# Performance work log

Hardware: AMD Instinct MI355X
Metric: run time of the kernel (lower is better)

Reference implementation:

```python
import jax, jax.numpy as jnp
from jax import lax
import numpy as np
import math

B, H, W, C = 4, 32, 256, 96
EXPAND, N, R, K = 2, 16, 6, 2
DI = EXPAND * C


def setup_inputs() -> dict:
    key = jax.random.key(0)
    ks = jax.random.split(key, 10)
    x = jax.random.normal(ks[0], (B, H, W, C), jnp.float32)
    W_in = jax.random.normal(ks[1], (2 * DI, C), jnp.float32) * (C ** -0.5)
    conv_w = jax.random.normal(ks[2], (DI, 1, 3, 3), jnp.float32) * (1.0 / 3.0)
    conv_b = jnp.zeros((DI,), jnp.float32)
    x_proj_weight = jax.random.normal(ks[3], (K, R + 2 * N, DI), jnp.float32) * (DI ** -0.5)
    dt_init_std = R ** -0.5
    dt_projs_weight = jax.random.uniform(ks[4], (K, DI, R), jnp.float32, -dt_init_std, dt_init_std)
    dt_min, dt_max = 1e-3, 1e-1
    dt = jnp.exp(jax.random.uniform(ks[5], (K, DI), jnp.float32) * (math.log(dt_max) - math.log(dt_min)) + math.log(dt_min))
    dt = jnp.clip(dt, 1e-4, None)
    dt_projs_bias = dt + jnp.log(-jnp.expm1(-dt))
    A_logs = jnp.tile(jnp.log(jnp.arange(1, N + 1, dtype=jnp.float32))[None, :], (K * DI, 1))
    Ds = jnp.ones((K * DI,), jnp.float32)
    W_out = jax.random.normal(ks[6], (C, DI), jnp.float32) * (DI ** -0.5)
    return {"x": x, "W_in": W_in, "conv_w": conv_w, "conv_b": conv_b,
            "x_proj_weight": x_proj_weight, "dt_projs_weight": dt_projs_weight,
            "dt_projs_bias": dt_projs_bias, "A_logs": A_logs, "Ds": Ds, "W_out": W_out}


def reference(x, W_in, conv_w, conv_b, x_proj_weight, dt_projs_weight,
              dt_projs_bias, A_logs, Ds, W_out):
    Bb, Hh, Ww, Cc = x.shape
    DIi = conv_w.shape[0]
    Kk = x_proj_weight.shape[0]
    Nn = A_logs.shape[-1]
    Rr = dt_projs_weight.shape[-1]
    L = Hh * Ww

    # in_proj + chunk
    xz = x @ W_in.T                       # (B,H,W,2*DI)
    xc, z = xz[..., :DIi], xz[..., DIi:]
    # depthwise conv (NCHW)
    xc = jnp.transpose(xc, (0, 3, 1, 2))
    xc = lax.conv_general_dilated(xc, conv_w, (1, 1), 'SAME',
                                  dimension_numbers=('NCHW', 'OIHW', 'NCHW'),
                                  feature_group_count=DIi)
    xc = jax.nn.silu(xc + conv_b[None, :, None, None])

    # cross-scan: forward + reversed (K=2)
    xf = xc.reshape(Bb, DIi, L)
    xs = jnp.stack([xf, xf[..., ::-1]], axis=1)          # (B,K,DI,L)

    x_dbl = jnp.einsum('bkdl,kcd->bkcl', xs, x_proj_weight)
    dts_r = x_dbl[:, :, :Rr]                             # (B,K,R,L)
    Bs = x_dbl[:, :, Rr:Rr + Nn]                         # (B,K,N,L)
    Cs = x_dbl[:, :, Rr + Nn:]                           # (B,K,N,L)
    dts = jnp.einsum('bkrl,kdr->bkdl', dts_r, dt_projs_weight)

    As = -jnp.exp(A_logs).reshape(Kk, DIi, Nn)           # (K,DI,N)
    Dd = Ds.reshape(Kk, DIi)
    delta = jax.nn.softplus(dts + dt_projs_bias.reshape(1, Kk, DIi, 1))

    # sequential selective scan over L
    u_t = jnp.moveaxis(xs, -1, 0)      # (L,B,K,DI)
    d_t = jnp.moveaxis(delta, -1, 0)   # (L,B,K,DI)
    B_t = jnp.moveaxis(Bs, -1, 0)      # (L,B,K,N)
    C_t = jnp.moveaxis(Cs, -1, 0)      # (L,B,K,N)

    def step(h, inp):
        u, dlt, Bt, Ct = inp
        dA = jnp.exp(dlt[..., None] * As)                       # (B,K,DI,N)
        h = dA * h + (dlt * u)[..., None] * Bt[:, :, None, :]
        y = jnp.sum(h * Ct[:, :, None, :], axis=-1)             # (B,K,DI)
        return h, y

    h0 = jnp.zeros((Bb, Kk, DIi, Nn), x.dtype)
    _, ys = lax.scan(step, h0, (u_t, d_t, B_t, C_t))
    ys = jnp.moveaxis(ys, 0, -1)                                # (B,K,DI,L)
    ys = ys + xs * Dd[None, :, :, None]

    # un-flip reversed direction and merge
    y = ys[:, 0] + ys[:, 1][..., ::-1]                          # (B,DI,L)
    y = jnp.transpose(y.reshape(Bb, DIi, Hh, Ww), (0, 2, 3, 1)) # (B,H,W,DI)

    out = (y * jax.nn.silu(z)) @ W_out.T                        # (B,H,W,C)
    return out
```

## Files before the change

### kernel.cpp

```cpp
#include <hip/hip_runtime.h>

constexpr int Bb = 4, Hh = 32, Wd = 256, Cc = 96;
constexpr int DI = 192, Nn = 16, Rr = 6, Kk = 2;
constexpr int LL = Hh * Wd;
constexpr int ROWS = Bb * LL;
constexpr int PROJ_C = 40;
constexpr int G = 128;
constexpr int CH = LL / G;
constexpr size_t YSZ = (size_t)Bb * DI * LL;

static __device__ __forceinline__ float sigmoidf_(float v) {
  return 1.f / (1.f + __expf(-v));
}

__global__ __launch_bounds__(256) void k_xz(const float* __restrict__ x,
                                            const float* __restrict__ Win,
                                            float* __restrict__ xc,
                                            float* __restrict__ zbuf) {
  __shared__ float As[32][132];
  __shared__ float Ws[32][100];
  const int tid = threadIdx.x;
  const int row0 = blockIdx.x * 128;
  const int c0 = blockIdx.y * 96;
  const int tx = tid & 7;
  const int ty = tid >> 3;
  float acc[4][12] = {};

  for (int kc = 0; kc < 3; ++kc) {
    const int d0 = kc * 32;
    __syncthreads();
    for (int v = tid; v < 1024; v += 256) {
      const int l = v >> 3, dk4 = v & 7;
      const float4 xv =
          *(const float4*)&x[(size_t)(row0 + l) * 96 + d0 + dk4 * 4];
      As[dk4 * 4 + 0][l] = xv.x;
      As[dk4 * 4 + 1][l] = xv.y;
      As[dk4 * 4 + 2][l] = xv.z;
      As[dk4 * 4 + 3][l] = xv.w;
    }
    for (int v = tid; v < 768; v += 256) {
      const int c = v >> 3, dk4 = v & 7;
      const float4 wv =
          *(const float4*)&Win[(size_t)(c0 + c) * 96 + d0 + dk4 * 4];
      Ws[dk4 * 4 + 0][c] = wv.x;
      Ws[dk4 * 4 + 1][c] = wv.y;
      Ws[dk4 * 4 + 2][c] = wv.z;
      Ws[dk4 * 4 + 3][c] = wv.w;
    }
    __syncthreads();
    for (int dk = 0; dk < 32; ++dk) {
      const float4 a4 = *(const float4*)&As[dk][ty * 4];
      const float4 w0 = *(const float4*)&Ws[dk][tx * 12];
      const float4 w1 = *(const float4*)&Ws[dk][tx * 12 + 4];
      const float4 w2 = *(const float4*)&Ws[dk][tx * 12 + 8];
      const float av[4] = {a4.x, a4.y, a4.z, a4.w};
      const float wv[12] = {w0.x, w0.y, w0.z, w0.w, w1.x, w1.y,
                            w1.z, w1.w, w2.x, w2.y, w2.z, w2.w};
#pragma unroll
      for (int i = 0; i < 4; ++i)
#pragma unroll
        for (int j = 0; j < 12; ++j)
          acc[i][j] = fmaf(av[i], wv[j], acc[i][j]);
    }
  }

  float* dst;
  int cc0;
  if (c0 < DI) { dst = xc; cc0 = c0; }
  else         { dst = zbuf; cc0 = c0 - DI; }
#pragma unroll
  for (int i = 0; i < 4; ++i) {
    float* op = dst + (size_t)(row0 + ty * 4 + i) * DI + cc0 + tx * 12;
    *(float4*)(op + 0) = make_float4(acc[i][0], acc[i][1], acc[i][2], acc[i][3]);
    *(float4*)(op + 4) = make_float4(acc[i][4], acc[i][5], acc[i][6], acc[i][7]);
    *(float4*)(op + 8) = make_float4(acc[i][8], acc[i][9], acc[i][10], acc[i][11]);
  }
}

__global__ __launch_bounds__(256) void k_conv(const float* __restrict__ xc,
                                              const float* __restrict__ cw,
                                              const float* __restrict__ cbias,
                                              float* __restrict__ xf) {
  __shared__ float wl[9 * DI];
  __shared__ float bl[DI];
  const int tid = threadIdx.x;
  for (int v = tid; v < 9 * DI; v += 256) {
    int dd = v / 9, t = v % 9;
    wl[t * DI + dd] = cw[v];
  }
  if (tid < DI) bl[tid] = cbias[tid];
  __syncthreads();

  int gid = blockIdx.x * 256 + tid;
  int d4 = gid % 48;
  int rem = gid / 48;
  int w4 = rem % 64;
  int bh = rem / 64;
  int h = bh % Hh, b = bh / Hh;
  const int d0 = d4 * 4, w0 = w4 * 4;

  float4 c[3][6];
#pragma unroll
  for (int dr = 0; dr < 3; ++dr) {
    const int h2 = h + dr - 1;
    const bool hv = (unsigned)h2 < (unsigned)Hh;
    const int hc = hv ? h2 : h;
    const float* rp = xc + ((size_t)(b * LL + (hc << 8))) * DI + d0;
#pragma unroll
    for (int j = 0; j < 6; ++j) {
      const int wc = w0 - 1 + j;
      const bool wv = (unsigned)wc < (unsigned)Wd;
      const int wcc = wv ? wc : w0;
      float4 v = *(const float4*)&rp[(size_t)wcc * DI];
      const float m = (hv && wv) ? 1.f : 0.f;
      c[dr][j] = make_float4(v.x * m, v.y * m, v.z * m, v.w * m);
    }
  }

  float4 wv9[9];
#pragma unroll
  for (int t = 0; t < 9; ++t) wv9[t] = *(const float4*)&wl[t * DI + d0];
  const float4 bias4 = *(const float4*)&bl[d0];

#pragma unroll
  for (int wi = 0; wi < 4; ++wi) {
    float4 a = bias4;
#pragma unroll
    for (int dr = 0; dr < 3; ++dr)
#pragma unroll
      for (int dc = 0; dc < 3; ++dc) {
        const float4 vv = c[dr][wi + dc];
        const float4 ww = wv9[dr * 3 + dc];
        a.x = fmaf(vv.x, ww.x, a.x);
        a.y = fmaf(vv.y, ww.y, a.y);
        a.z = fmaf(vv.z, ww.z, a.z);
        a.w = fmaf(vv.w, ww.w, a.w);
      }
    float4 r;
    r.x = a.x * sigmoidf_(a.x);
    r.y = a.y * sigmoidf_(a.y);
    r.z = a.z * sigmoidf_(a.z);
    r.w = a.w * sigmoidf_(a.w);
    *(float4*)&xf[((size_t)(b * LL + (h << 8) + w0 + wi)) * DI + d0] = r;
  }
}

__global__ __launch_bounds__(256) void k_proj(const float* __restrict__ xf,
                                              const float* __restrict__ xpw,
                                              float* __restrict__ proj) {
  __shared__ float smem[5376];
  float* As = smem;
  float* Ws = smem + 32 * 68;
  const int tid = threadIdx.x;
  const int row0 = blockIdx.x * 64;
  const int b = row0 >> 13;
  const int l0 = row0 & (LL - 1);
  const int tx = tid & 15;
  const int ty = tid >> 4;
  float acc[4][5] = {};

  for (int kc = 0; kc < 6; ++kc) {
    const int d0 = kc * 32;
    __syncthreads();
    for (int v = tid; v < 512; v += 256) {
      const int l = v >> 3, dk4 = v & 7;
      const float4 xv =
          *(const float4*)&xf[((size_t)b * LL + l0 + l) * DI + d0 + dk4 * 4];
      As[(dk4 * 4 + 0) * 68 + l] = xv.x;
      As[(dk4 * 4 + 1) * 68 + l] = xv.y;
      As[(dk4 * 4 + 2) * 68 + l] = xv.z;
      As[(dk4 * 4 + 3) * 68 + l] = xv.w;
    }
    for (int v = tid; v < 640; v += 256) {
      const int s = v >> 3, dk4 = v & 7;
      const int k = s / 40, off = s % 40;
      float4 wv = make_float4(0.f, 0.f, 0.f, 0.f);
      if (off < 6 || off >= 8) {
        const int c = off < 6 ? off : off - 2;
        wv = *(const float4*)&xpw[(size_t)(k * 38 + c) * DI + d0 + dk4 * 4];
      }
      Ws[(dk4 * 4 + 0) * 84 + s] = wv.x;
      Ws[(dk4 * 4 + 1) * 84 + s] = wv.y;
      Ws[(dk4 * 4 + 2) * 84 + s] = wv.z;
      Ws[(dk4 * 4 + 3) * 84 + s] = wv.w;
    }
    __syncthreads();
    for (int dk = 0; dk < 32; ++dk) {
      const float4 a4 = *(const float4*)&As[dk * 68 + ty * 4];
      float w[5];
#pragma unroll
      for (int j = 0; j < 5; ++j) w[j] = Ws[dk * 84 + tx * 5 + j];
      const float av[4] = {a4.x, a4.y, a4.z, a4.w};
#pragma unroll
      for (int i = 0; i < 4; ++i)
#pragma unroll
        for (int j = 0; j < 5; ++j)
          acc[i][j] = fmaf(av[i], w[j], acc[i][j]);
    }
  }

  __syncthreads();
  float* res = smem;
#pragma unroll
  for (int i = 0; i < 4; ++i)
#pragma unroll
    for (int j = 0; j < 5; ++j)
      res[(ty * 4 + i) * 84 + tx * 5 + j] = acc[i][j];
  __syncthreads();
#pragma unroll
  for (int k = 0; k < 2; ++k) {
    float* dst = proj + ((size_t)(b * Kk + k) * LL + l0) * PROJ_C;
    for (int v = tid; v < 640; v += 256) {
      const int l = v / 10, q = v % 10;
      *(float4*)&dst[l * PROJ_C + q * 4] =
          *(const float4*)&res[l * 84 + k * 40 + q * 4];
    }
  }
}

struct St {
  float4 p0;
  float2 p1;
  float u;
  float4 Bv[4];
  float4 Cv[4];
};

template <int PASS>
static __device__ __forceinline__ void load_st(St& S,
                                               const float* __restrict__ pr,
                                               const float* __restrict__ up) {
  S.p0 = *(const float4*)pr;
  S.p1 = *(const float2*)(pr + 4);
#pragma unroll
  for (int j = 0; j < 4; ++j) S.Bv[j] = *(const float4*)(pr + 8 + 4 * j);
  if (PASS == 3) {
#pragma unroll
    for (int j = 0; j < 4; ++j) S.Cv[j] = *(const float4*)(pr + 24 + 4 * j);
  }
  S.u = *up;
}

template <int PASS>
static __device__ __forceinline__ void step_compute(
    const St& S, float (&h)[16], const float (&w6)[6], const float dbias,
    const float Dv, float& dsum, float* __restrict__ yw) {
  float vr = dbias;
  vr = fmaf(S.p0.x, w6[0], vr);
  vr = fmaf(S.p0.y, w6[1], vr);
  vr = fmaf(S.p0.z, w6[2], vr);
  vr = fmaf(S.p0.w, w6[3], vr);
  vr = fmaf(S.p1.x, w6[4], vr);
  vr = fmaf(S.p1.y, w6[5], vr);
  const float ex = __expf(vr);
  const float dlt = (vr > 20.f) ? vr : __logf(1.f + ex);
  const float E = __expf(-dlt);
  if (PASS == 1) dsum += dlt;
  const float du = dlt * S.u;
  const float E2 = E * E, E4 = E2 * E2, E8 = E4 * E4;
  const float fbs[4] = {E, E4 * E, E8 * E, E8 * E4 * E};

  if (PASS == 3) {
    float yp = 0.f, yq = 0.f;
#pragma unroll
    for (int j = 0; j < 4; ++j) {
      float f = fbs[j];
      const float4 Bj = S.Bv[j];
      const float4 Cj = S.Cv[j];
      h[4 * j + 0] = fmaf(f, h[4 * j + 0], du * Bj.x);
      yp = fmaf(h[4 * j + 0], Cj.x, yp);
      f *= E;
      h[4 * j + 1] = fmaf(f, h[4 * j + 1], du * Bj.y);
      yq = fmaf(h[4 * j + 1], Cj.y, yq);
      f *= E;
      h[4 * j + 2] = fmaf(f, h[4 * j + 2], du * Bj.z);
      yp = fmaf(h[4 * j + 2], Cj.z, yp);
      f *= E;
      h[4 * j + 3] = fmaf(f, h[4 * j + 3], du * Bj.w);
      yq = fmaf(h[4 * j + 3], Cj.w, yq);
    }
    *yw = fmaf(S.u, Dv, yp + yq);
  } else {
#pragma unroll
    for (int j = 0; j < 4; ++j) {
      float f = fbs[j];
      const float4 Bj = S.Bv[j];
      h[4 * j + 0] = fmaf(f, h[4 * j + 0], du * Bj.x);
      f *= E;
      h[4 * j + 1] = fmaf(f, h[4 * j + 1], du * Bj.y);
      f *= E;
      h[4 * j + 2] = fmaf(f, h[4 * j + 2], du * Bj.z);
      f *= E;
      h[4 * j + 3] = fmaf(f, h[4 * j + 3], du * Bj.w);
    }
  }
}

template <int PASS, int KDIR>
static __device__ __forceinline__ void scan_wave(
    const float* __restrict__ proj, const float* __restrict__ xf,
    const float* __restrict__ dtw, const float* __restrict__ dtb,
    const float* __restrict__ Dsv, const float* __restrict__ hinit,
    float* __restrict__ hend, float* __restrict__ Pst,
    float* __restrict__ yout, const int b, const int g, const int d) {
  constexpr int PRS = KDIR ? -PROJ_C : PROJ_C;
  constexpr int DIS = KDIR ? -DI : DI;
  const int kd = KDIR * DI + d;
  const int bk = b * Kk + KDIR;

  float w6[6];
#pragma unroll
  for (int r = 0; r < 6; ++r) w6[r] = dtw[kd * 6 + r];
  const float dbias = dtb[kd];
  const float Dv = (PASS == 3) ? Dsv[kd] : 0.f;

  const size_t hbase = (((size_t)(bk * G + g)) * DI + d) * Nn;
  float h[16];
  if (PASS == 1) {
#pragma unroll
    for (int n = 0; n < 16; ++n) h[n] = 0.f;
  } else {
#pragma unroll
    for (int j = 0; j < 4; ++j) {
      const float4 h4 = *(const float4*)&hinit[hbase + 4 * j];
      h[4 * j + 0] = h4.x;
      h[4 * j + 1] = h4.y;
      h[4 * j + 2] = h4.z;
      h[4 * j + 3] = h4.w;
    }
  }

  const int l0 = KDIR ? (LL - 1 - g * CH) : (g * CH);
  const float* pr = proj + ((size_t)bk * LL + l0) * PROJ_C;
  const float* up = xf + ((size_t)b * LL + l0) * DI + d;
  float* yw = yout + (size_t)KDIR * YSZ + ((size_t)b * LL + l0) * DI + d;

  float dsum = 0.f;
  St S0, S1;
  load_st<PASS>(S0, pr, up);
  pr += PRS;
  up += DIS;

  for (int t = 0; t < CH; t += 2) {
    load_st<PASS>(S1, pr, up);
    pr += PRS;
    up += DIS;
    step_compute<PASS>(S0, h, w6, dbias, Dv, dsum, yw);
    if (PASS == 3) yw += DIS;
    load_st<PASS>(S0, pr, up);
    pr += PRS;
    up += DIS;
    step_compute<PASS>(S1, h, w6, dbias, Dv, dsum, yw);
    if (PASS == 3) yw += DIS;
  }

  if (PASS == 1) {
    const float Es = __expf(-dsum);
    const float Es2 = Es * Es, Es4 = Es2 * Es2, Es8 = Es4 * Es4;
    const float qbs[4] = {Es, Es4 * Es, Es8 * Es, Es8 * Es4 * Es};
#pragma unroll
    for (int j = 0; j < 4; ++j) {
      float f = qbs[j];
      float4 pv;
      pv.x = f; f *= Es;
      pv.y = f; f *= Es;
      pv.z = f; f *= Es;
      pv.w = f;
      *(float4*)&Pst[hbase + 4 * j] = pv;
      *(float4*)&hend[hbase + 4 * j] =
          make_float4(h[4 * j], h[4 * j + 1], h[4 * j + 2], h[4 * j + 3]);
    }
  }
}

template <int PASS>
__global__ __launch_bounds__(256) void k_scan(
    const float* __restrict__ proj, const float* __restrict__ xf,
    const float* __restrict__ dtw, const float* __restrict__ dtb,
    const float* __restrict__ Dsv, const float* __restrict__ hinit,
    float* __restrict__ hend, float* __restrict__ Pst,
    float* __restrict__ yout) {
  const int lane = threadIdx.x & 63;
  const int wid = blockIdx.x * 4 + (threadIdx.x >> 6);
  const int kdir = wid & 1;
  int w2 = wid >> 1;
  const int dt3 = w2 % 3;
  w2 /= 3;
  const int g = w2 & (G - 1);
  const int b = w2 >> 7;
  const int d = dt3 * 64 + lane;

  if (kdir == 0)
    scan_wave<PASS, 0>(proj, xf, dtw, dtb, Dsv, hinit, hend, Pst, yout, b, g,
                       d);
  else
    scan_wave<PASS, 1>(proj, xf, dtw, dtb, Dsv, hinit, hend, Pst, yout, b, g,
                       d);
}

__global__ __launch_bounds__(256) void k_scan2(const float* __restrict__ hend,
                                               const float* __restrict__ Pst,
                                               float* __restrict__ hini) {
  int idx = blockIdx.x * 256 + threadIdx.x;
  int n = idx & 15;
  int rem = idx >> 4;
  int d = rem % DI;
  int bk = rem / DI;
  float carry = 0.f;
#pragma unroll 8
  for (int g = 0; g < G; ++g) {
    size_t a = (((size_t)(bk * G + g)) * DI + d) * Nn + n;
    float hv = hend[a], pv = Pst[a];
    hini[a] = carry;
    carry = fmaf(pv, carry, hv);
  }
}

__global__ __launch_bounds__(256) void k_out(const float* __restrict__ y,
                                             const float* __restrict__ zbuf,
                                             const float* __restrict__ Wout,
                                             float* __restrict__ out) {
  __shared__ float As[32][132];
  __shared__ float Ws[32][100];
  const int tid = threadIdx.x;
  const int row0 = blockIdx.x * 128;
  const int b = row0 >> 13;
  const int l0 = row0 & (LL - 1);
  const int tx = tid & 7;
  const int ty = tid >> 3;
  float acc[4][12] = {};

  for (int kc = 0; kc < 6; ++kc) {
    const int d0 = kc * 32;
    __syncthreads();
    for (int v = tid; v < 1024; v += 256) {
      const int l = v >> 3, dk4 = v & 7;
      const size_t idx = ((size_t)b * LL + l0 + l) * DI + d0 + dk4 * 4;
      const float4 zv = *(const float4*)&zbuf[idx];
      const float4 y0v = *(const float4*)&y[idx];
      const float4 y1v = *(const float4*)&y[YSZ + idx];
      As[dk4 * 4 + 0][l] = zv.x * sigmoidf_(zv.x) * (y0v.x + y1v.x);
      As[dk4 * 4 + 1][l] = zv.y * sigmoidf_(zv.y) * (y0v.y + y1v.y);
      As[dk4 * 4 + 2][l] = zv.z * sigmoidf_(zv.z) * (y0v.z + y1v.z);
      As[dk4 * 4 + 3][l] = zv.w * sigmoidf_(zv.w) * (y0v.w + y1v.w);
    }
    for (int v = tid; v < 768; v += 256) {
      const int c = v >> 3, dk4 = v & 7;
      const float4 wv = *(const float4*)&Wout[(size_t)c * DI + d0 + dk4 * 4];
      Ws[dk4 * 4 + 0][c] = wv.x;
      Ws[dk4 * 4 + 1][c] = wv.y;
      Ws[dk4 * 4 + 2][c] = wv.z;
      Ws[dk4 * 4 + 3][c] = wv.w;
    }
    __syncthreads();
    for (int dk = 0; dk < 32; ++dk) {
      const float4 a4 = *(const float4*)&As[dk][ty * 4];
      const float4 w0 = *(const float4*)&Ws[dk][tx * 12];
      const float4 w1 = *(const float4*)&Ws[dk][tx * 12 + 4];
      const float4 w2 = *(const float4*)&Ws[dk][tx * 12 + 8];
      const float av[4] = {a4.x, a4.y, a4.z, a4.w};
      const float wv[12] = {w0.x, w0.y, w0.z, w0.w, w1.x, w1.y,
                            w1.z, w1.w, w2.x, w2.y, w2.z, w2.w};
#pragma unroll
      for (int i = 0; i < 4; ++i)
#pragma unroll
        for (int j = 0; j < 12; ++j)
          acc[i][j] = fmaf(av[i], wv[j], acc[i][j]);
    }
  }

#pragma unroll
  for (int i = 0; i < 4; ++i) {
    float* op = out + ((size_t)b * LL + l0 + ty * 4 + i) * 96 + tx * 12;
    *(float4*)(op + 0) = make_float4(acc[i][0], acc[i][1], acc[i][2], acc[i][3]);
    *(float4*)(op + 4) = make_float4(acc[i][4], acc[i][5], acc[i][6], acc[i][7]);
    *(float4*)(op + 8) = make_float4(acc[i][8], acc[i][9], acc[i][10], acc[i][11]);
  }
}

extern "C" void kernel_launch(void* const* d_in, const int* in_sizes, int n_in,
                              void* d_out, int out_size, void* d_ws,
                              size_t ws_size, hipStream_t stream) {
  const float* x    = (const float*)d_in[0];
  const float* Win  = (const float*)d_in[1];
  const float* cw   = (const float*)d_in[2];
  const float* cb   = (const float*)d_in[3];
  const float* xpw  = (const float*)d_in[4];
  const float* dtw  = (const float*)d_in[5];
  const float* dtb  = (const float*)d_in[6];
  const float* Dsv  = (const float*)d_in[8];
  const float* Wout = (const float*)d_in[9];
  float* out = (float*)d_out;

  float* ws = (float*)d_ws;
  size_t o = 0;
  float* zbuf  = ws + o;  o += (size_t)ROWS * DI;
  float* xf    = ws + o;  o += (size_t)ROWS * DI;
  float* proj  = ws + o;  o += (size_t)Bb * Kk * LL * PROJ_C;
  const size_t hsz = (size_t)Bb * Kk * G * DI * Nn;
  float* hend = ws + o;  o += hsz;
  float* Pst  = ws + o;  o += hsz;
  float* hini = ws + o;  o += hsz;
  float* y    = ws + o;  o += 2 * YSZ;
  float* xc   = y;

  k_xz<<<dim3(ROWS / 128, 4), 256, 0, stream>>>(x, Win, xc, zbuf);
  k_conv<<<dim3((Bb * Hh * 64 * 48) / 256), 256, 0, stream>>>(xc, cw, cb, xf);
  k_proj<<<dim3(ROWS / 64), 256, 0, stream>>>(xf, xpw, proj);
  k_scan<1><<<dim3(Bb * Kk * G * 3 / 4), 256, 0, stream>>>(
      proj, xf, dtw, dtb, Dsv, nullptr, hend, Pst, nullptr);
  k_scan2<<<dim3((Bb * Kk * DI * Nn) / 256), 256, 0, stream>>>(hend, Pst,
                                                               hini);
  k_scan<3><<<dim3(Bb * Kk * G * 3 / 4), 256, 0, stream>>>(
      proj, xf, dtw, dtb, Dsv, hini, nullptr, nullptr, y);
  k_out<<<dim3(ROWS / 128), 256, 0, stream>>>(y, zbuf, Wout, out);
}
```

Measured before the change: 337.6 us.

## Stage scan inputs through double-buffered shared memory per 192-thread block

The chunked selective-scan kernels now run one 192-thread block per (batch, direction, chunk), with all DI channels in one block. Each block cooperatively loads 16-step sub-chunks of the projection rows and u values into double-buffered LDS with coalesced float4 loads and prefetches the next sub-chunk into registers. This replaces per-thread redundant global loads of the same proj row by every lane. Pass 1 loads only the first 24 columns. The cost is block-wide barriers every 16 steps and a smaller block size.

```diff
diff --git a/kernel.cpp b/kernel.cpp
--- a/kernel.cpp
+++ b/kernel.cpp
@@ -218,95 +218,25 @@
   }
 }
 
-struct St {
-  float4 p0;
-  float2 p1;
-  float u;
-  float4 Bv[4];
-  float4 Cv[4];
-};
-
-template <int PASS>
-static __device__ __forceinline__ void load_st(St& S,
-                                               const float* __restrict__ pr,
-                                               const float* __restrict__ up) {
-  S.p0 = *(const float4*)pr;
-  S.p1 = *(const float2*)(pr + 4);
-#pragma unroll
-  for (int j = 0; j < 4; ++j) S.Bv[j] = *(const float4*)(pr + 8 + 4 * j);
-  if (PASS == 3) {
-#pragma unroll
-    for (int j = 0; j < 4; ++j) S.Cv[j] = *(const float4*)(pr + 24 + 4 * j);
-  }
-  S.u = *up;
-}
-
-template <int PASS>
-static __device__ __forceinline__ void step_compute(
-    const St& S, float (&h)[16], const float (&w6)[6], const float dbias,
-    const float Dv, float& dsum, float* __restrict__ yw) {
-  float vr = dbias;
-  vr = fmaf(S.p0.x, w6[0], vr);
-  vr = fmaf(S.p0.y, w6[1], vr);
-  vr = fmaf(S.p0.z, w6[2], vr);
-  vr = fmaf(S.p0.w, w6[3], vr);
-  vr = fmaf(S.p1.x, w6[4], vr);
-  vr = fmaf(S.p1.y, w6[5], vr);
-  const float ex = __expf(vr);
-  const float dlt = (vr > 20.f) ? vr : __logf(1.f + ex);
-  const float E = __expf(-dlt);
-  if (PASS == 1) dsum += dlt;
-  const float du = dlt * S.u;
-  const float E2 = E * E, E4 = E2 * E2, E8 = E4 * E4;
-  const float fbs[4] = {E, E4 * E, E8 * E, E8 * E4 * E};
-
-  if (PASS == 3) {
-    float yp = 0.f, yq = 0.f;
-#pragma unroll
-    for (int j = 0; j < 4; ++j) {
-      float f = fbs[j];
-      const float4 Bj = S.Bv[j];
-      const float4 Cj = S.Cv[j];
-      h[4 * j + 0] = fmaf(f, h[4 * j + 0], du * Bj.x);
-      yp = fmaf(h[4 * j + 0], Cj.x, yp);
-      f *= E;
-      h[4 * j + 1] = fmaf(f, h[4 * j + 1], du * Bj.y);
-      yq = fmaf(h[4 * j + 1], Cj.y, yq);
-      f *= E;
-      h[4 * j + 2] = fmaf(f, h[4 * j + 2], du * Bj.z);
-      yp = fmaf(h[4 * j + 2], Cj.z, yp);
-      f *= E;
-      h[4 * j + 3] = fmaf(f, h[4 * j + 3], du * Bj.w);
-      yq = fmaf(h[4 * j + 3], Cj.w, yq);
-    }
-    *yw = fmaf(S.u, Dv, yp + yq);
-  } else {
-#pragma unroll
-    for (int j = 0; j < 4; ++j) {
-      float f = fbs[j];
-      const float4 Bj = S.Bv[j];
-      h[4 * j + 0] = fmaf(f, h[4 * j + 0], du * Bj.x);
-      f *= E;
-      h[4 * j + 1] = fmaf(f, h[4 * j + 1], du * Bj.y);
-      f *= E;
-      h[4 * j + 2] = fmaf(f, h[4 * j + 2], du * Bj.z);
-      f *= E;
-      h[4 * j + 3] = fmaf(f, h[4 * j + 3], du * Bj.w);
-    }
-  }
-}
-
 template <int PASS, int KDIR>
-static __device__ __forceinline__ void scan_wave(
+static __device__ __forceinline__ void scan_block(
+    float* __restrict__ pb, float* __restrict__ ub,
     const float* __restrict__ proj, const float* __restrict__ xf,
     const float* __restrict__ dtw, const float* __restrict__ dtb,
     const float* __restrict__ Dsv, const float* __restrict__ hinit,
     float* __restrict__ hend, float* __restrict__ Pst,
-    float* __restrict__ yout, const int b, const int g, const int d) {
-  constexpr int PRS = KDIR ? -PROJ_C : PROJ_C;
+    float* __restrict__ yout, const int b, const int g) {
+  constexpr int RC = (PASS == 3) ? PROJ_C : 24;
+  constexpr int SUB = 16;
+  constexpr int NSUB = CH / SUB;
   constexpr int DIS = KDIR ? -DI : DI;
+  const int tid = threadIdx.x;
+  const int lane = tid & 63;
+  const int wv = tid >> 6;
+  const int d = wv * 64 + lane;
   const int kd = KDIR * DI + d;
   const int bk = b * Kk + KDIR;
+  const int l0 = KDIR ? (LL - 1 - g * CH) : (g * CH);
 
   float w6[6];
 #pragma unroll
@@ -330,28 +260,113 @@
     }
   }
 
-  const int l0 = KDIR ? (LL - 1 - g * CH) : (g * CH);
-  const float* pr = proj + ((size_t)bk * LL + l0) * PROJ_C;
-  const float* up = xf + ((size_t)b * LL + l0) * DI + d;
   float* yw = yout + (size_t)KDIR * YSZ + ((size_t)b * LL + l0) * DI + d;
 
+  float4 preg = make_float4(0.f, 0.f, 0.f, 0.f);
+  float4 ureg[4];
+
+  auto span = [&](int s) {
+    return KDIR ? (l0 - SUB * s - (SUB - 1)) : (l0 + SUB * s);
+  };
+  auto issue = [&](int s) {
+    const size_t pbase = ((size_t)bk * LL + span(s)) * PROJ_C;
+    const size_t ubase = ((size_t)b * LL + span(s)) * DI;
+    if (PASS == 3) {
+      if (tid < 160) preg = *(const float4*)&proj[pbase + tid * 4];
+    } else {
+      if (tid < 96) {
+        const int i = tid / 6, c4 = tid % 6;
+        preg = *(const float4*)&proj[pbase + i * PROJ_C + c4 * 4];
+      }
+    }
+#pragma unroll
+    for (int r = 0; r < 4; ++r)
+      ureg[r] = *(const float4*)&xf[ubase + (tid + 192 * r) * 4];
+  };
+  auto commit = [&](int buf) {
+    if (PASS == 3) {
+      if (tid < 160) {
+        const int i = (tid * 4) / PROJ_C, c = (tid * 4) % PROJ_C;
+        const int li = (KDIR ? (SUB - 1 - i) : i) * RC + c;
+        *(float4*)&pb[buf * (SUB * RC) + li] = preg;
+      }
+    } else {
+      if (tid < 96) {
+        const int i = tid / 6, c = (tid % 6) * 4;
+        const int li = (KDIR ? (SUB - 1 - i) : i) * RC + c;
+        *(float4*)&pb[buf * (SUB * RC) + li] = preg;
+      }
+    }
+#pragma unroll
+    for (int r = 0; r < 4; ++r) {
+      const int f4 = tid + 192 * r;
+      const int i = f4 / 48, c = (f4 % 48) * 4;
+      const int li = (KDIR ? (SUB - 1 - i) : i) * DI + c;
+      *(float4*)&ub[buf * (SUB * DI) + li] = ureg[r];
+    }
+  };
+
   float dsum = 0.f;
-  St S0, S1;
-  load_st<PASS>(S0, pr, up);
-  pr += PRS;
-  up += DIS;
-
-  for (int t = 0; t < CH; t += 2) {
-    load_st<PASS>(S1, pr, up);
-    pr += PRS;
-    up += DIS;
-    step_compute<PASS>(S0, h, w6, dbias, Dv, dsum, yw);
-    if (PASS == 3) yw += DIS;
-    load_st<PASS>(S0, pr, up);
-    pr += PRS;
-    up += DIS;
-    step_compute<PASS>(S1, h, w6, dbias, Dv, dsum, yw);
-    if (PASS == 3) yw += DIS;
+  issue(0);
+  commit(0);
+  __syncthreads();
+  issue(1);
+
+  for (int s = 0; s < NSUB; ++s) {
+    const int cur = s & 1;
+    const float* Pb = pb + cur * (SUB * RC);
+    const float* Ub = ub + cur * (SUB * DI) + d;
+#pragma unroll
+    for (int t = 0; t < SUB; ++t) {
+      const float* P = Pb + t * RC;
+      const float u = Ub[t * DI];
+      const float4 p0 = *(const float4*)P;
+      const float2 p1 = *(const float2*)(P + 4);
+      float vr = dbias;
+      vr = fmaf(p0.x, w6[0], vr);
+      vr = fmaf(p0.y, w6[1], vr);
+      vr = fmaf(p0.z, w6[2], vr);
+      vr = fmaf(p0.w, w6[3], vr);
+      vr = fmaf(p1.x, w6[4], vr);
+      vr = fmaf(p1.y, w6[5], vr);
+      const float ex = __expf(vr);
+      const float dlt = (vr > 20.f) ? vr : __logf(1.f + ex);
+      const float E = __expf(-dlt);
+      if (PASS == 1) dsum += dlt;
+      const float du = dlt * u;
+      const float E2 = E * E, E4 = E2 * E2, E8 = E4 * E4;
+      const float fbs[4] = {E, E4 * E, E8 * E, E8 * E4 * E};
+      float yp = 0.f, yq = 0.f;
+#pragma unroll
+      for (int j = 0; j < 4; ++j) {
+        float f = fbs[j];
+        const float4 Bj = *(const float4*)(P + 8 + 4 * j);
+        h[4 * j + 0] = fmaf(f, h[4 * j + 0], du * Bj.x);
+        f *= E;
+        h[4 * j + 1] = fmaf(f, h[4 * j + 1], du * Bj.y);
+        f *= E;
+        h[4 * j + 2] = fmaf(f, h[4 * j + 2], du * Bj.z);
+        f *= E;
+        h[4 * j + 3] = fmaf(f, h[4 * j + 3], du * Bj.w);
+        if (PASS == 3) {
+          const float4 Cj = *(const float4*)(P + 24 + 4 * j);
+          yp = fmaf(h[4 * j + 0], Cj.x, yp);
+          yq = fmaf(h[4 * j + 1], Cj.y, yq);
+          yp = fmaf(h[4 * j + 2], Cj.z, yp);
+          yq = fmaf(h[4 * j + 3], Cj.w, yq);
+        }
+      }
+      if (PASS == 3) {
+        *yw = fmaf(u, Dv, yp + yq);
+        yw += DIS;
+      }
+    }
+    __syncthreads();
+    if (s + 1 < NSUB) {
+      commit((s + 1) & 1);
+      if (s + 2 < NSUB) issue(s + 2);
+      __syncthreads();
+    }
   }
 
   if (PASS == 1) {
@@ -374,28 +389,28 @@
 }
 
 template <int PASS>
-__global__ __launch_bounds__(256) void k_scan(
+__global__ __launch_bounds__(192) void k_scan(
     const float* __restrict__ proj, const float* __restrict__ xf,
     const float* __restrict__ dtw, const float* __restrict__ dtb,
     const float* __restrict__ Dsv, const float* __restrict__ hinit,
     float* __restrict__ hend, float* __restrict__ Pst,
     float* __restrict__ yout) {
-  const int lane = threadIdx.x & 63;
-  const int wid = blockIdx.x * 4 + (threadIdx.x >> 6);
-  const int kdir = wid & 1;
-  int w2 = wid >> 1;
-  const int dt3 = w2 % 3;
-  w2 /= 3;
-  const int g = w2 & (G - 1);
-  const int b = w2 >> 7;
-  const int d = dt3 * 64 + lane;
+  constexpr int RC = (PASS == 3) ? PROJ_C : 24;
+  __shared__ float pbuf[2 * 16 * RC];
+  __shared__ float ubuf[2 * 16 * DI];
+  int bid = blockIdx.x;
+  const int kdir = bid & 1;
+  bid >>= 1;
+  const int g = bid & (G - 1);
+  bid >>= 7;
+  const int b = bid;
 
   if (kdir == 0)
-    scan_wave<PASS, 0>(proj, xf, dtw, dtb, Dsv, hinit, hend, Pst, yout, b, g,
-                       d);
+    scan_block<PASS, 0>(pbuf, ubuf, proj, xf, dtw, dtb, Dsv, hinit, hend, Pst,
+                        yout, b, g);
   else
-    scan_wave<PASS, 1>(proj, xf, dtw, dtb, Dsv, hinit, hend, Pst, yout, b, g,
-                       d);
+    scan_block<PASS, 1>(pbuf, ubuf, proj, xf, dtw, dtb, Dsv, hinit, hend, Pst,
+                        yout, b, g);
 }
 
 __global__ __launch_bounds__(256) void k_scan2(const float* __restrict__ hend,
@@ -507,11 +522,11 @@
   k_xz<<<dim3(ROWS / 128, 4), 256, 0, stream>>>(x, Win, xc, zbuf);
   k_conv<<<dim3((Bb * Hh * 64 * 48) / 256), 256, 0, stream>>>(xc, cw, cb, xf);
   k_proj<<<dim3(ROWS / 64), 256, 0, stream>>>(xf, xpw, proj);
-  k_scan<1><<<dim3(Bb * Kk * G * 3 / 4), 256, 0, stream>>>(
+  k_scan<1><<<dim3(Bb * Kk * G), 192, 0, stream>>>(
       proj, xf, dtw, dtb, Dsv, nullptr, hend, Pst, nullptr);
   k_scan2<<<dim3((Bb * Kk * DI * Nn) / 256), 256, 0, stream>>>(hend, Pst,
                                                                hini);
-  k_scan<3><<<dim3(Bb * Kk * G * 3 / 4), 256, 0, stream>>>(
+  k_scan<3><<<dim3(Bb * Kk * G), 192, 0, stream>>>(
       proj, xf, dtw, dtb, Dsv, hini, nullptr, nullptr, y);
   k_out<<<dim3(ROWS / 128), 256, 0, stream>>>(y, zbuf, Wout, out);
 }
```

Measured after the change: 335.7 us. No clear change (-0.6%).
